# Kernel tuning notes

Hardware: AMD Instinct MI355X
Metric: run time of the kernel (lower is better)

Reference implementation:

```python
import jax, jax.numpy as jnp
import numpy as np

K = 11        # filter_size
HALF = K // 2 # 5
N_ITER = 5
EPS = 1e-8


def setup_inputs() -> dict:
    key = jax.random.key(0)
    k1, k2 = jax.random.split(key)
    logits = jax.random.normal(k1, (16, 100000), dtype=jnp.float32)
    p = jax.random.normal(k2, (16, 100000, 3), dtype=jnp.float32)
    return {"logits": logits, "p": p}


def _shift_stack(x, offsets, n):
    # x: [B, C, N+2*HALF] padded; returns [B, len(offsets), C, N]
    return jnp.stack([x[:, :, d:d + n] for d in offsets], axis=1)


def reference(logits, p):
    B, N = logits.shape
    feat = jnp.transpose(p, (0, 2, 1))      # [B,3,N]  (p.permute(0,2,1))
    unary = logits[:, None, :]              # [B,1,N]  (logits.unsqueeze(1))

    offsets = [d for d in range(K) if d != HALF]  # exclude self-connection

    fpad = jnp.pad(feat, ((0, 0), (0, 0), (HALF, HALF)))
    mpad = jnp.pad(jnp.ones((B, 1, N), logits.dtype), ((0, 0), (0, 0), (HALF, HALF)))
    f_sh = _shift_stack(fpad, offsets, N)   # [B,10,3,N]
    m_sh = _shift_stack(mpad, offsets, N)   # [B,10,1,N] valid mask (zero outside seq)

    # Gaussian pairwise kernel on point features, fixed across iterations
    w = jnp.exp(-0.5 * jnp.sum((feat[:, None] - f_sh) ** 2, axis=2, keepdims=True)) * m_sh  # [B,10,1,N]
    wsum = jnp.sum(w, axis=1) + EPS         # [B,1,N]

    def body(q, _):
        qpad = jnp.pad(q, ((0, 0), (0, 0), (HALF, HALF)))
        q_sh = _shift_stack(qpad, offsets, N)          # [B,10,1,N]
        msg = jnp.sum(w * q_sh, axis=1) / wsum          # normalized message
        q_new = jax.nn.sigmoid(unary + msg)             # mean-field update
        return q_new, None

    q0 = jax.nn.sigmoid(unary)
    q, _ = jax.lax.scan(body, q0, None, length=N_ITER)
    return q[:, 0, :]  # .squeeze() -> [B,N] marginal probabilities
```

## Files before the change

kernel.cpp:

```cpp
#include <hip/hip_runtime.h>


constexpr int BLK   = 64;
constexpr int G     = 8;
constexpr int E     = BLK * G;
constexpr int HALF_ = 5;
constexpr int NITER = 5;
constexpr int R     = HALF_ * NITER;
constexpr int C     = E - 2 * R;
constexpr int NSEG  = E / 4;
constexpr float EPS = 1e-8f;

__device__ __forceinline__ float frcp(float x) { return __builtin_amdgcn_rcpf(x); }
__device__ __forceinline__ float sigm(float x) { return frcp(1.0f + __expf(-x)); }
__device__ __forceinline__ int   swz(int seg)  { return seg ^ ((seg >> 3) & 7); }

__global__ __launch_bounds__(BLK, 3) void crf_kernel(
    const float* __restrict__ logits, const float* __restrict__ p,
    float* __restrict__ out, int N, int chunks_per_b)
{
  __shared__ float4 s_q4[NSEG];

  const int b     = blockIdx.x / chunks_per_b;
  const int chunk = blockIdx.x % chunks_per_b;
  const int s0    = chunk * C - R;
  const int t     = threadIdx.x;
  const int base  = G * t;
  const int gb    = s0 + base;
  const float* lg = logits + (size_t)b * N;
  const float* pp = p + (size_t)b * N * 3;

  float f[18][3];
  #pragma unroll
  for (int i = 0; i < 18; ++i) {
    int g  = gb + i - 5;
    int gc = min(max(g, 0), N - 1);
    const float* src = pp + 3 * (size_t)gc;
    f[i][0] = src[0]; f[i][1] = src[1]; f[i][2] = src[2];
  }

  float upe[13][5];
  #pragma unroll
  for (int i = 0; i < 13; ++i) {
    int g = gb + i - 5;
    #pragma unroll
    for (int d = 0; d < 5; ++d) {
      float d0 = f[i][0] - f[i + d + 1][0];
      float d1 = f[i][1] - f[i + d + 1][1];
      float d2 = f[i][2] - f[i + d + 1][2];
      float ex = __expf(-0.5f * (d0 * d0 + d1 * d1 + d2 * d2));
      bool valid = (g >= 0) && (g + d + 1 < N);
      upe[i][d] = valid ? ex : 0.0f;
    }
  }

  float wl[G][5], wr[G][5], un[G], q[G];
  #pragma unroll
  for (int k = 0; k < G; ++k) {
    int i = k + 5;
    float ws = EPS;
    #pragma unroll
    for (int d = 0; d < 5; ++d) ws += upe[i][d] + upe[i - d - 1][d];
    float inv = frcp(ws);
    #pragma unroll
    for (int d = 0; d < 5; ++d) {
      wr[k][d] = upe[i][d] * inv;
      wl[k][d] = upe[i - d - 1][d] * inv;
    }
    int g  = gb + k;
    int gc = min(max(g, 0), N - 1);
    float u = lg[gc];
    un[k] = u;
    q[k]  = sigm(u);
  }

  const int sgA  = swz(2 * t);
  const int sgB  = swz(2 * t + 1);
  const int sgL0 = swz(max(2 * t - 2, 0));
  const int sgL1 = swz(max(2 * t - 1, 0));
  const int sgR0 = swz(min(2 * t + 2, NSEG - 1));
  const int sgR1 = swz(min(2 * t + 3, NSEG - 1));

  s_q4[sgA] = make_float4(q[0], q[1], q[2], q[3]);
  s_q4[sgB] = make_float4(q[4], q[5], q[6], q[7]);
  __syncthreads();

  #pragma unroll
  for (int it = 0; it < NITER; ++it) {
    float4 L0 = s_q4[sgL0];
    float4 L1 = s_q4[sgL1];
    float4 R0 = s_q4[sgR0];
    float4 R1 = s_q4[sgR1];
    float qx[18];
    qx[0] = L0.w; qx[1] = L1.x; qx[2] = L1.y; qx[3] = L1.z; qx[4] = L1.w;
    #pragma unroll
    for (int k = 0; k < G; ++k) qx[5 + k] = q[k];
    qx[13] = R0.x; qx[14] = R0.y; qx[15] = R0.z; qx[16] = R0.w; qx[17] = R1.x;

    #pragma unroll
    for (int k = 0; k < G; ++k) {
      float msg = 0.0f;
      #pragma unroll
      for (int d = 0; d < 5; ++d) {
        msg += wl[k][d] * qx[5 + k - d - 1];
        msg += wr[k][d] * qx[5 + k + d + 1];
      }
      q[k] = sigm(un[k] + msg);
    }

    if (it != NITER - 1) {
      __syncthreads();
      s_q4[sgA] = make_float4(q[0], q[1], q[2], q[3]);
      s_q4[sgB] = make_float4(q[4], q[5], q[6], q[7]);
      __syncthreads();
    }
  }

  #pragma unroll
  for (int k = 0; k < G; ++k) {
    int e = base + k;
    int g = s0 + e;
    if (e >= R && e < E - R && g < N) out[(size_t)b * N + g] = q[k];
  }
}

extern "C" void kernel_launch(void* const* d_in, const int* in_sizes, int n_in,
                              void* d_out, int out_size, void* d_ws, size_t ws_size,
                              hipStream_t stream) {
  const float* logits = (const float*)d_in[0];
  const float* p      = (const float*)d_in[1];
  float* out          = (float*)d_out;
  const int N = 100000;
  const int B = in_sizes[0] / N;
  const int chunks_per_b = (N + C - 1) / C;
  dim3 grid(B * chunks_per_b), block(BLK);
  crf_kernel<<<grid, block, 0, stream>>>(logits, p, out, N, chunks_per_b);
}
```

Before: 18.91 us.

## Stage features and logits through LDS with coalesced loads and vectorized stores

Feature and logit loads now go through shared memory: each thread loads strided elements into swizzled LDS, so global reads are coalesced instead of each thread gathering 18 overlapping points. Pairwise exp weights are computed once per pair from a sliding window, and the redundant upe array is removed. The halo grows from 25 to 28 so outputs align to float4, and output stores become float4. The cost is extra LDS traffic, one more barrier, and slightly more halo recompute per chunk.

Measured after the change: 23.26 us. 1.23x slower.

```diff
diff --git a/kernel.cpp b/kernel.cpp
--- a/kernel.cpp
+++ b/kernel.cpp
@@ -4,82 +4,103 @@
 constexpr int BLK   = 64;
 constexpr int G     = 8;
 constexpr int E     = BLK * G;
-constexpr int HALF_ = 5;
+constexpr int HL    = 28;
+constexpr int C     = E - 2 * HL;
 constexpr int NITER = 5;
-constexpr int R     = HALF_ * NITER;
-constexpr int C     = E - 2 * R;
-constexpr int NSEG  = E / 4;
+constexpr int OF    = 8;
+constexpr int FE    = E + 2 * OF;
+constexpr int NSEGQ = E / 4;
 constexpr float EPS = 1e-8f;
 
 __device__ __forceinline__ float frcp(float x) { return __builtin_amdgcn_rcpf(x); }
 __device__ __forceinline__ float sigm(float x) { return frcp(1.0f + __expf(-x)); }
-__device__ __forceinline__ int   swz(int seg)  { return seg ^ ((seg >> 3) & 7); }
+__device__ __forceinline__ int   swzseg(int s) { return s ^ ((s >> 3) & 7); }
+__device__ __forceinline__ int   swzd(int d)   { int s = d >> 2; return (swzseg(s) << 2) | (d & 3); }
 
 __global__ __launch_bounds__(BLK, 3) void crf_kernel(
     const float* __restrict__ logits, const float* __restrict__ p,
     float* __restrict__ out, int N, int chunks_per_b)
 {
-  __shared__ float4 s_q4[NSEG];
+  __shared__ float4 s_f4[FE];
+  __shared__ float  s_lg[E];
+  __shared__ float4 s_q4[NSEGQ];
 
   const int b     = blockIdx.x / chunks_per_b;
   const int chunk = blockIdx.x % chunks_per_b;
-  const int s0    = chunk * C - R;
+  const int s0    = chunk * C - HL;
   const int t     = threadIdx.x;
   const int base  = G * t;
   const int gb    = s0 + base;
   const float* lg = logits + (size_t)b * N;
   const float* pp = p + (size_t)b * N * 3;
 
-  float f[18][3];
   #pragma unroll
-  for (int i = 0; i < 18; ++i) {
-    int g  = gb + i - 5;
-    int gc = min(max(g, 0), N - 1);
-    const float* src = pp + 3 * (size_t)gc;
-    f[i][0] = src[0]; f[i][1] = src[1]; f[i][2] = src[2];
+  for (int jp = 0; jp < 9; ++jp) {
+    int idx = 64 * jp + t;
+    if (idx < FE) {
+      int g  = s0 + idx - OF;
+      int gc = min(max(g, 0), N - 1);
+      const float* src = pp + 3 * (size_t)gc;
+      s_f4[swzseg(idx)] = make_float4(src[0], src[1], src[2], 0.0f);
+    }
+  }
+  #pragma unroll
+  for (int jl = 0; jl < 8; ++jl) {
+    int idx = 64 * jl + t;
+    int g   = s0 + idx;
+    int gc  = min(max(g, 0), N - 1);
+    s_lg[swzd(idx)] = lg[gc];
+  }
+  __syncthreads();
+
+  float wr[G][5], wl[G][5];
+  float4 win[6];
+  #pragma unroll
+  for (int j = 0; j < 5; ++j) win[j] = s_f4[swzseg(base - 5 + j + OF)];
+  #pragma unroll
+  for (int i = 0; i < 13; ++i) {
+    win[(i + 5) % 6] = s_f4[swzseg(base + i + OF)];
+    const float4 a = win[i % 6];
+    const int g = gb + i - 5;
+    #pragma unroll
+    for (int d = 0; d < 5; ++d) {
+      const float4 bb = win[(i + d + 1) % 6];
+      float d0 = a.x - bb.x, d1 = a.y - bb.y, d2 = a.z - bb.z;
+      float ex = __expf(-0.5f * (d0 * d0 + d1 * d1 + d2 * d2));
+      bool valid = (g >= 0) && (g + d + 1 < N);
+      ex = valid ? ex : 0.0f;
+      if (i >= 5) wr[i - 5][d] = ex;
+      const int kl = i + d - 4;
+      if (kl >= 0 && kl < G) wl[kl][d] = ex;
+    }
+  }
+  #pragma unroll
+  for (int k = 0; k < G; ++k) {
+    float ws = EPS;
+    #pragma unroll
+    for (int d = 0; d < 5; ++d) ws += wr[k][d] + wl[k][d];
+    float inv = frcp(ws);
+    #pragma unroll
+    for (int d = 0; d < 5; ++d) { wr[k][d] *= inv; wl[k][d] *= inv; }
   }
 
-  float upe[13][5];
-  #pragma unroll
-  for (int i = 0; i < 13; ++i) {
-    int g = gb + i - 5;
+  float un[G], q[G];
+  {
+    const float4* lg4 = (const float4*)s_lg;
+    float4 u0 = lg4[swzseg(2 * t)];
+    float4 u1 = lg4[swzseg(2 * t + 1)];
+    un[0] = u0.x; un[1] = u0.y; un[2] = u0.z; un[3] = u0.w;
+    un[4] = u1.x; un[5] = u1.y; un[6] = u1.z; un[7] = u1.w;
     #pragma unroll
-    for (int d = 0; d < 5; ++d) {
-      float d0 = f[i][0] - f[i + d + 1][0];
-      float d1 = f[i][1] - f[i + d + 1][1];
-      float d2 = f[i][2] - f[i + d + 1][2];
-      float ex = __expf(-0.5f * (d0 * d0 + d1 * d1 + d2 * d2));
-      bool valid = (g >= 0) && (g + d + 1 < N);
-      upe[i][d] = valid ? ex : 0.0f;
-    }
+    for (int k = 0; k < G; ++k) q[k] = sigm(un[k]);
   }
 
-  float wl[G][5], wr[G][5], un[G], q[G];
-  #pragma unroll
-  for (int k = 0; k < G; ++k) {
-    int i = k + 5;
-    float ws = EPS;
-    #pragma unroll
-    for (int d = 0; d < 5; ++d) ws += upe[i][d] + upe[i - d - 1][d];
-    float inv = frcp(ws);
-    #pragma unroll
-    for (int d = 0; d < 5; ++d) {
-      wr[k][d] = upe[i][d] * inv;
-      wl[k][d] = upe[i - d - 1][d] * inv;
-    }
-    int g  = gb + k;
-    int gc = min(max(g, 0), N - 1);
-    float u = lg[gc];
-    un[k] = u;
-    q[k]  = sigm(u);
-  }
-
-  const int sgA  = swz(2 * t);
-  const int sgB  = swz(2 * t + 1);
-  const int sgL0 = swz(max(2 * t - 2, 0));
-  const int sgL1 = swz(max(2 * t - 1, 0));
-  const int sgR0 = swz(min(2 * t + 2, NSEG - 1));
-  const int sgR1 = swz(min(2 * t + 3, NSEG - 1));
+  const int sgA  = swzseg(2 * t);
+  const int sgB  = swzseg(2 * t + 1);
+  const int sgL0 = swzseg(max(2 * t - 2, 0));
+  const int sgL1 = swzseg(max(2 * t - 1, 0));
+  const int sgR0 = swzseg(min(2 * t + 2, NSEGQ - 1));
+  const int sgR1 = swzseg(min(2 * t + 3, NSEGQ - 1));
 
   s_q4[sgA] = make_float4(q[0], q[1], q[2], q[3]);
   s_q4[sgB] = make_float4(q[4], q[5], q[6], q[7]);
@@ -116,11 +137,21 @@
     }
   }
 
+  float* ob = out + (size_t)b * N;
   #pragma unroll
-  for (int k = 0; k < G; ++k) {
-    int e = base + k;
-    int g = s0 + e;
-    if (e >= R && e < E - R && g < N) out[(size_t)b * N + g] = q[k];
+  for (int h = 0; h < 2; ++h) {
+    const int e0 = base + 4 * h;
+    if (e0 >= HL && e0 + 4 <= E - HL) {
+      const int gidx = chunk * C + (e0 - HL);
+      float4 v = make_float4(q[4 * h], q[4 * h + 1], q[4 * h + 2], q[4 * h + 3]);
+      if (gidx + 3 < N) {
+        *(float4*)(ob + gidx) = v;
+      } else {
+        #pragma unroll
+        for (int j = 0; j < 4; ++j)
+          if (gidx + j < N) ob[gidx + j] = (&v.x)[j];
+      }
+    }
   }
 }
 
```
